# Performance work log

Measured on AMD Instinct MI355X. Metric: run time of the kernel, lower is better.

## Reference

```python
import jax, jax.numpy as jnp
import numpy as np
from jax import lax

B, T, N, F, K = 8, 16, 1024, 128, 4


def setup_inputs() -> dict:
    key = jax.random.key(0)
    k1, k2, k3, k4 = jax.random.split(key, 4)
    x = jax.random.normal(k1, (B, T, N, F), dtype=jnp.float32)
    # shift operator scaled so its spectral radius is ~1 (stable powers L^1..L^K)
    L = jax.random.normal(k2, (N, N), dtype=jnp.float32) / jnp.sqrt(jnp.float32(N))
    # xavier_uniform with relu gain: limit = gain * sqrt(6/(fan_in+fan_out))
    gain = jnp.sqrt(jnp.float32(2.0))
    lim = gain * jnp.sqrt(6.0 / (F + F))
    W = jax.random.uniform(k3, (K, F, F), dtype=jnp.float32, minval=-lim, maxval=lim)
    H = jax.random.uniform(k4, (K, F, F), dtype=jnp.float32, minval=-lim, maxval=lim)
    return {"x": x, "L": L, "W": W, "H": H}


def reference(x, L, W, H):
    """Recurrent graph-polynomial filter.

    h_t = relu( sum_{k=0}^{K-1} L^{k+1} @ (x_t @ W[k] + h_{t-1} @ H[k]) ), h_{-1}=0.
    Matches the torch loop where alpha_k starts at L and is multiplied by L each tap.
    """
    Kt = W.shape[0]
    # powers L^1 .. L^K, stacked [K, N, N]
    pows = [L]
    for _ in range(1, Kt):
        pows.append(pows[-1] @ L)
    Lp = jnp.stack(pows)

    def step(h, x_t):
        # x_t, h: [B, N, F]
        s = jnp.einsum('bnf,kfg->kbng', x_t, W) + jnp.einsum('bnf,kfg->kbng', h, H)
        z = jnp.einsum('knm,kbmg->bng', Lp, s)
        h_new = jax.nn.relu(z)
        return h_new, h_new

    xT = jnp.swapaxes(x, 0, 1)          # [T, B, N, F]
    h0 = jnp.zeros_like(x[:, 0])        # [B, N, F]
    _, outs = lax.scan(step, h0, xT)    # [T, B, N, F]
    return jnp.swapaxes(outs, 0, 1)     # [B, T, N, F]
```

## Files before the change

### kernel.cpp

```cpp
#include <hip/hip_runtime.h>
#include <stdint.h>


typedef __bf16 bf16_t;
typedef __bf16 bf16x4 __attribute__((ext_vector_type(4)));
typedef __bf16 bf16x8 __attribute__((ext_vector_type(8)));
typedef float  f32x4  __attribute__((ext_vector_type(4)));

__device__ __forceinline__ void gload_lds16(const void* g, void* l) {
    __builtin_amdgcn_global_load_lds(
        (const __attribute__((address_space(1))) void*)g,
        (__attribute__((address_space(3))) void*)l,
        16, 0, 0);
}

template<int N> __device__ __forceinline__ void wait_vmcnt() {
    if constexpr (N == 0)       asm volatile("s_waitcnt vmcnt(0)" ::: "memory");
    else if constexpr (N == 2)  asm volatile("s_waitcnt vmcnt(2)" ::: "memory");
    else if constexpr (N == 4)  asm volatile("s_waitcnt vmcnt(4)" ::: "memory");
    else if constexpr (N == 6)  asm volatile("s_waitcnt vmcnt(6)" ::: "memory");
    else if constexpr (N == 8)  asm volatile("s_waitcnt vmcnt(8)" ::: "memory");
    else                        asm volatile("s_waitcnt vmcnt(16)" ::: "memory");
}


__global__ void k_convert_x(const float* __restrict__ xin,
                            bf16_t* __restrict__ xb, int n4) {
    int i = blockIdx.x * 256 + threadIdx.x;
    int stride = gridDim.x * 256;
    for (; i < n4; i += stride) {
        float4 v = reinterpret_cast<const float4*>(xin)[i];
        bf16x4 o = { (bf16_t)v.x, (bf16_t)v.y, (bf16_t)v.z, (bf16_t)v.w };
        reinterpret_cast<bf16x4*>(xb)[i] = o;
    }
}

__global__ void k_setup_L(const float* __restrict__ L,
                          bf16_t* __restrict__ Lcat,
                          bf16_t* __restrict__ Lt) {
    int idx = blockIdx.x * 256 + threadIdx.x;
    int n = idx >> 10, m = idx & 1023;
    float v = L[idx];
    Lcat[n * 4096 + m] = (bf16_t)v;
    Lt[m * 1024 + n]   = (bf16_t)v;
}

__global__ void k_setup_WH(const float* __restrict__ W,
                           const float* __restrict__ H,
                           bf16_t* __restrict__ WHT) {
    int idx = blockIdx.x * 256 + threadIdx.x;
    int k = idx >> 14, f = (idx >> 7) & 127, g = idx & 127;
    WHT[(k * 128 + g) * 256 + f]       = (bf16_t)W[idx];
    WHT[(k * 128 + g) * 256 + 128 + f] = (bf16_t)H[idx];
}


__global__ __launch_bounds__(256)
void k_combine8(const bf16_t* __restrict__ Zp,
                bf16_t* __restrict__ h, float* __restrict__ out, int t) {
    int i = blockIdx.x * 256 + threadIdx.x;
    int n  = i >> 7;
    int c8 = (i & 127) * 8;
    size_t o = (size_t)n * 1024 + c8;
    float s[8] = {};
    #pragma unroll
    for (int z = 0; z < 8; ++z) {
        bf16x8 v = *reinterpret_cast<const bf16x8*>(Zp + (size_t)z * 1048576 + o);
        #pragma unroll
        for (int j = 0; j < 8; ++j) s[j] += (float)v[j];
    }
    bf16x8 hb;
    float4 o0, o1;
    #pragma unroll
    for (int j = 0; j < 8; ++j) {
        s[j] = fmaxf(s[j], 0.f);
        hb[j] = (bf16_t)s[j];
    }
    o0.x = s[0]; o0.y = s[1]; o0.z = s[2]; o0.w = s[3];
    o1.x = s[4]; o1.y = s[5]; o1.z = s[6]; o1.w = s[7];
    int b = c8 >> 7, g = c8 & 127;
    *reinterpret_cast<bf16x8*>(h + (size_t)b * 131072 + (size_t)n * 128 + g) = hb;
    float* op = out + (size_t)b * 2097152 + (size_t)t * 131072
                    + (size_t)n * 128 + g;
    *reinterpret_cast<float4*>(op)     = o0;
    *reinterpret_cast<float4*>(op + 4) = o1;
}

template<int BM, int BN, int GX, int GY, int GZ, int KTOT,
         int EPI, int BADDR, int ZK, int DEC, int NBUF>
__device__ __forceinline__
void gemm_body(const bf16_t* __restrict__ A, int lda,
               const bf16_t* __restrict__ BT, int ldbt,
               const bf16_t* __restrict__ B2,
               bf16_t* __restrict__ Cb, float* __restrict__ Cf,
               int ldc, int t)
{
    constexpr int BK = 64;
    constexpr int WM = BM / 2, WN = BN / 2;
    constexpr int MF = WM / 16, NF = WN / 16;
    constexpr int NT = KTOT / BK;
    constexpr int NWG = GX * GY * GZ;
    constexpr int ACH = BM * 8;
    constexpr int BCH = BN * 8;
    constexpr int LPT = (ACH + BCH) / 256;

    __shared__ __align__(16) bf16_t As[NBUF][BM * BK];
    __shared__ __align__(16) bf16_t Bs[NBUF][BN * BK];

    const int tid  = threadIdx.x;
    const int lane = tid & 63;
    const int wave = tid >> 6;
    const int wm = wave >> 1, wn = wave & 1;

    const int id  = blockIdx.x;
    const int swz = (id & 7) * (NWG / 8) + (id >> 3);
    int bx, by, bz;
    if (DEC == 0) {
        bx = swz % GX; by = (swz / GX) % GY; bz = swz / (GX * GY);
    } else {
        by = swz % GY; bz = (swz / GY) % GZ; bx = swz / (GY * GZ);
    }

    const int m0 = by * BM;
    const int c0 = bx * BN;
    const int kb_ = bz;

    const bf16_t* Ap = (EPI == 1) ? (A + kb_ * 128 * 256) : A;

    f32x4 acc[MF][NF] = {};

    auto stage = [&](int bufi, int kt) {
        const int q0 = kt * BK + (ZK > 0 ? kb_ * ZK : 0);
        #pragma unroll
        for (int i = 0; i < ACH / 256; ++i) {
            int chunk = i * 256 + tid;
            int off = chunk * 16;
            int row = off >> 7;
            int kel = ((off ^ ((row & 7) << 4)) & 127) >> 1;
            const bf16_t* src = Ap + (size_t)(m0 + row) * lda + (q0 + kel);
            gload_lds16(src, (char*)(&As[bufi][0]) + off);
        }
        #pragma unroll
        for (int i = 0; i < BCH / 256; ++i) {
            int chunk = i * 256 + tid;
            int off = chunk * 16;
            int row = off >> 7;
            int kel = ((off ^ ((row & 7) << 4)) & 127) >> 1;
            int c = c0 + row;
            const bf16_t* src;
            if (BADDR == 0) {
                src = BT + (size_t)c * ldbt + (q0 + kel);
            } else {
                int f = q0 + kel;
                if (q0 < 128) {
                    src = BT + (size_t)(c >> 10) * 2097152
                             + (size_t)t * 131072
                             + (size_t)(c & 1023) * 128 + f;
                } else {
                    src = B2 + (size_t)c * 128 + (f - 128);
                }
            }
            gload_lds16(src, (char*)(&Bs[bufi][0]) + off);
        }
    };

    auto compute = [&](int cur) {
        #pragma unroll
        for (int kk = 0; kk < 2; ++kk) {
            bf16x8 af[MF], bfr[NF];
            const int klane = (kk * 32 + (lane >> 4) * 8) * 2;
            #pragma unroll
            for (int mf = 0; mf < MF; ++mf) {
                int row = wm * WM + mf * 16 + (lane & 15);
                int bo = (row * 128 + klane) ^ ((row & 7) << 4);
                af[mf] = *reinterpret_cast<const bf16x8*>(
                             (const char*)(&As[cur][0]) + bo);
            }
            #pragma unroll
            for (int nf = 0; nf < NF; ++nf) {
                int row = wn * WN + nf * 16 + (lane & 15);
                int bo = (row * 128 + klane) ^ ((row & 7) << 4);
                bfr[nf] = *reinterpret_cast<const bf16x8*>(
                              (const char*)(&Bs[cur][0]) + bo);
            }
            #pragma unroll
            for (int mf = 0; mf < MF; ++mf)
                #pragma unroll
                for (int nf = 0; nf < NF; ++nf)
                    acc[mf][nf] = __builtin_amdgcn_mfma_f32_16x16x32_bf16(
                        af[mf], bfr[nf], acc[mf][nf], 0, 0, 0);
        }
    };

    if constexpr (NBUF == 3) {
        stage(0, 0);
        stage(1, 1);
        for (int kt = 0; kt < NT; ++kt) {
            if (kt < NT - 1) wait_vmcnt<LPT>(); else wait_vmcnt<0>();
            __builtin_amdgcn_s_barrier();
            __builtin_amdgcn_sched_barrier(0);
            if (kt + 2 < NT) stage((kt + 2) % 3, kt + 2);
            compute(kt % 3);
            __builtin_amdgcn_sched_barrier(0);
        }
    } else {
        stage(0, 0);
        stage(1, 1);
        for (int kt = 0; kt < NT; ++kt) {
            if (kt > 0 && kt + 1 < NT) {
                __builtin_amdgcn_s_barrier();
                stage((kt + 1) & 1, kt + 1);
            }
            if (kt + 1 < NT) wait_vmcnt<LPT>();
            else             wait_vmcnt<0>();
            __builtin_amdgcn_s_barrier();
            __builtin_amdgcn_sched_barrier(0);
            compute(kt & 1);
            __builtin_amdgcn_sched_barrier(0);
        }
    }

    #pragma unroll
    for (int mf = 0; mf < MF; ++mf) {
        #pragma unroll
        for (int nf = 0; nf < NF; ++nf) {
            f32x4 v = acc[mf][nf];
            int col   = c0 + wn * WN + nf * 16 + (lane & 15);
            int rbase = m0 + wm * WM + mf * 16 + ((lane >> 4) * 4);
            #pragma unroll
            for (int r = 0; r < 4; ++r) {
                int row = rbase + r;
                float val = v[r];
                if (EPI == 0) {
                    Cb[(size_t)row * ldc + col] = (bf16_t)val;
                } else if (EPI == 1) {
                    Cb[(size_t)(col >> 10) * 524288 + (size_t)row * 4096
                       + (size_t)kb_ * 1024 + (col & 1023)] = (bf16_t)val;
                } else if (EPI == 2) {
                    val = fmaxf(val, 0.f);
                    int b = col >> 7, g = col & 127;
                    Cb[(size_t)b * 131072 + (size_t)row * 128 + g] = (bf16_t)val;
                    Cf[(size_t)b * 2097152 + (size_t)t * 131072
                       + (size_t)row * 128 + g] = val;
                } else {
                    Cb[(size_t)kb_ * 1048576 + (size_t)row * 1024 + col]
                        = (bf16_t)val;
                }
            }
        }
    }
}


__global__ __launch_bounds__(256)
void k_chain(const bf16_t* __restrict__ A, const bf16_t* __restrict__ BT,
             bf16_t* __restrict__ Cb) {
    gemm_body<64, 64, 16, 16, 1, 1024, 0, 0, 0, 0, 3>(
        A, 4096, BT, 1024, nullptr, Cb, nullptr, 4096, 0);
}

__global__ __launch_bounds__(256)
void k_feat(const bf16_t* __restrict__ WHT, const bf16_t* __restrict__ xb,
            const bf16_t* __restrict__ h, bf16_t* __restrict__ Sbuf, int t) {
    gemm_body<128, 64, 128, 1, 4, 256, 1, 1, 0, 1, 3>(
        WHT, 256, xb, 0, h, Sbuf, nullptr, 0, t);
}

__global__ __launch_bounds__(256)
void k_graph(const bf16_t* __restrict__ Lcat, const bf16_t* __restrict__ Sbuf,
             bf16_t* __restrict__ Zp) {
    gemm_body<128, 128, 8, 8, 8, 512, 3, 0, 512, 0, 2>(
        Lcat, 4096, Sbuf, 4096, nullptr, Zp, nullptr, 0, 0);
}

__global__ __launch_bounds__(256)
void k_graph_ns(const bf16_t* __restrict__ Lcat, const bf16_t* __restrict__ Sbuf,
                bf16_t* __restrict__ h, float* __restrict__ out, int t) {
    gemm_body<128, 128, 8, 8, 1, 4096, 2, 0, 0, 0, 3>(
        Lcat, 4096, Sbuf, 4096, nullptr, h, out, 0, t);
}


extern "C" void kernel_launch(void* const* d_in, const int* in_sizes, int n_in,
                              void* d_out, int out_size, void* d_ws, size_t ws_size,
                              hipStream_t stream) {
    const float* x = (const float*)d_in[0];
    const float* L = (const float*)d_in[1];
    const float* W = (const float*)d_in[2];
    const float* H = (const float*)d_in[3];
    float* out = (float*)d_out;

    char* ws = (char*)d_ws;
    bf16_t* xb   = (bf16_t*)(ws);
    bf16_t* Lcat = (bf16_t*)(ws + 33554432);
    bf16_t* Lt   = (bf16_t*)(ws + 41943040);
    bf16_t* WHT  = (bf16_t*)(ws + 44040192);
    bf16_t* Sbuf = (bf16_t*)(ws + 44302336);
    bf16_t* h    = (bf16_t*)(ws + 52690944);
    bf16_t* Zp   = (bf16_t*)(ws + 54788096);
    if (ws_size < 54788096u) return;
    const bool bigws = (ws_size >= 71565312u);

    hipMemsetAsync(h, 0, 2097152, stream);
    k_convert_x<<<4096, 256, 0, stream>>>(x, xb, 16777216 / 4);
    k_setup_L <<<4096, 256, 0, stream>>>(L, Lcat, Lt);
    k_setup_WH<<<256, 256, 0, stream>>>(W, H, WHT);

    for (int p = 1; p < 4; ++p) {
        k_chain<<<256, 256, 0, stream>>>(Lcat + (p - 1) * 1024, Lt,
                                         Lcat + p * 1024);
    }

    for (int t = 0; t < 16; ++t) {
        k_feat<<<512, 256, 0, stream>>>(WHT, xb, h, Sbuf, t);
        if (bigws) {
            k_graph<<<512, 256, 0, stream>>>(Lcat, Sbuf, Zp);
            k_combine8<<<512, 256, 0, stream>>>(Zp, h, out, t);
        } else {
            k_graph_ns<<<64, 256, 0, stream>>>(Lcat, Sbuf, h, out, t);
        }
    }
}
```

Before: 503.8 us.

## Fuse split-K combine into feature GEMM and merge setup kernels

The per-step combine kernel (summing split-K partials, ReLU, writing h and output) is folded into the prologue of a new fused feature-transform kernel. That kernel builds the h tile directly in LDS and runs the W/H projection with a 3-stage async pipeline. The three setup kernels and the memset are merged into one launch. This removes 15 launches plus the global round trip of h per timestep, but the new kernel uses 256 blocks instead of 512 and recomputes the combine inside the GEMM.

```diff
diff --git a/kernel.cpp b/kernel.cpp
--- a/kernel.cpp
+++ b/kernel.cpp
@@ -17,6 +17,7 @@
 template<int N> __device__ __forceinline__ void wait_vmcnt() {
     if constexpr (N == 0)       asm volatile("s_waitcnt vmcnt(0)" ::: "memory");
     else if constexpr (N == 2)  asm volatile("s_waitcnt vmcnt(2)" ::: "memory");
+    else if constexpr (N == 3)  asm volatile("s_waitcnt vmcnt(3)" ::: "memory");
     else if constexpr (N == 4)  asm volatile("s_waitcnt vmcnt(4)" ::: "memory");
     else if constexpr (N == 6)  asm volatile("s_waitcnt vmcnt(6)" ::: "memory");
     else if constexpr (N == 8)  asm volatile("s_waitcnt vmcnt(8)" ::: "memory");
@@ -24,34 +25,30 @@
 }
 
 
-__global__ void k_convert_x(const float* __restrict__ xin,
-                            bf16_t* __restrict__ xb, int n4) {
-    int i = blockIdx.x * 256 + threadIdx.x;
-    int stride = gridDim.x * 256;
-    for (; i < n4; i += stride) {
-        float4 v = reinterpret_cast<const float4*>(xin)[i];
-        bf16x4 o = { (bf16_t)v.x, (bf16_t)v.y, (bf16_t)v.z, (bf16_t)v.w };
-        reinterpret_cast<bf16x4*>(xb)[i] = o;
-    }
-}
-
-__global__ void k_setup_L(const float* __restrict__ L,
-                          bf16_t* __restrict__ Lcat,
-                          bf16_t* __restrict__ Lt) {
-    int idx = blockIdx.x * 256 + threadIdx.x;
-    int n = idx >> 10, m = idx & 1023;
-    float v = L[idx];
-    Lcat[n * 4096 + m] = (bf16_t)v;
-    Lt[m * 1024 + n]   = (bf16_t)v;
-}
-
-__global__ void k_setup_WH(const float* __restrict__ W,
-                           const float* __restrict__ H,
-                           bf16_t* __restrict__ WHT) {
-    int idx = blockIdx.x * 256 + threadIdx.x;
-    int k = idx >> 14, f = (idx >> 7) & 127, g = idx & 127;
-    WHT[(k * 128 + g) * 256 + f]       = (bf16_t)W[idx];
-    WHT[(k * 128 + g) * 256 + 128 + f] = (bf16_t)H[idx];
+__global__ void k_setup(const float* __restrict__ x, const float* __restrict__ L,
+                        const float* __restrict__ W, const float* __restrict__ H,
+                        bf16_t* __restrict__ xb, bf16_t* __restrict__ Lcat,
+                        bf16_t* __restrict__ Lt, bf16_t* __restrict__ WHT) {
+    int bid = blockIdx.x;
+    if (bid < 4096) {
+        int idx = bid * 256 + threadIdx.x;
+        int n = idx >> 10, m = idx & 1023;
+        float v = L[idx];
+        Lcat[n * 4096 + m] = (bf16_t)v;
+        Lt[m * 1024 + n]   = (bf16_t)v;
+    } else if (bid < 4352) {
+        int idx = (bid - 4096) * 256 + threadIdx.x;
+        int k = idx >> 14, f = (idx >> 7) & 127, g = idx & 127;
+        WHT[(k * 128 + g) * 256 + f]       = (bf16_t)W[idx];
+        WHT[(k * 128 + g) * 256 + 128 + f] = (bf16_t)H[idx];
+    } else {
+        int i = (bid - 4352) * 256 + threadIdx.x;
+        for (; i < 4194304; i += 4096 * 256) {
+            float4 v = reinterpret_cast<const float4*>(x)[i];
+            bf16x4 o = { (bf16_t)v.x, (bf16_t)v.y, (bf16_t)v.z, (bf16_t)v.w };
+            reinterpret_cast<bf16x4*>(xb)[i] = o;
+        }
+    }
 }
 
 
@@ -72,10 +69,7 @@
     bf16x8 hb;
     float4 o0, o1;
     #pragma unroll
-    for (int j = 0; j < 8; ++j) {
-        s[j] = fmaxf(s[j], 0.f);
-        hb[j] = (bf16_t)s[j];
-    }
+    for (int j = 0; j < 8; ++j) { s[j] = fmaxf(s[j], 0.f); hb[j] = (bf16_t)s[j]; }
     o0.x = s[0]; o0.y = s[1]; o0.z = s[2]; o0.w = s[3];
     o1.x = s[4]; o1.y = s[5]; o1.z = s[6]; o1.w = s[7];
     int b = c8 >> 7, g = c8 & 127;
@@ -84,6 +78,163 @@
                     + (size_t)n * 128 + g;
     *reinterpret_cast<float4*>(op)     = o0;
     *reinterpret_cast<float4*>(op + 4) = o1;
+}
+
+template<bool FIRST>
+__global__ __launch_bounds__(256)
+void k_fused(const bf16_t* __restrict__ WHT, const bf16_t* __restrict__ xb,
+             const bf16_t* __restrict__ Zp, bf16_t* __restrict__ Sbuf,
+             float* __restrict__ out, int t)
+{
+    __shared__ __align__(16) bf16_t BsF[4 * 32 * 64];
+    __shared__ __align__(16) bf16_t AsF[3 * 128 * 64];
+
+    const int tid  = threadIdx.x;
+    const int lane = tid & 63;
+    const int wave = tid >> 6;
+    const int wm = wave >> 1, wn = wave & 1;
+
+    const int id = blockIdx.x;
+    const int bx = (id & 7) * 32 + (id >> 3);
+    const int c0 = bx * 32;
+    const int b  = c0 >> 10;
+    const int mb = c0 & 1023;
+
+    #pragma unroll
+    for (int ks = 0; ks < 2; ++ks) {
+        int off = tid * 16;
+        int row = off >> 7;
+        int kel = ((off ^ ((row & 7) << 4)) & 127) >> 1;
+        const bf16_t* src = xb + (size_t)b * 2097152 + (size_t)t * 131072
+                          + (size_t)(mb + row) * 128 + ks * 64 + kel;
+        gload_lds16(src, (char*)BsF + ks * 4096 + off);
+    }
+    auto stageA = [&](int bufi, int s) {
+        const int k = s >> 2, st = s & 3;
+        #pragma unroll
+        for (int i = 0; i < 4; ++i) {
+            int chunk = i * 256 + tid;
+            int off = chunk * 16;
+            int row = off >> 7;
+            int kel = ((off ^ ((row & 7) << 4)) & 127) >> 1;
+            const bf16_t* src = WHT + (size_t)(k * 128 + row) * 256
+                              + st * 64 + kel;
+            gload_lds16(src, (char*)AsF + bufi * 16384 + off);
+        }
+    };
+    stageA(0, 0);
+    stageA(1, 1);
+
+    {
+        const int r  = tid >> 3;
+        const int g0 = (tid & 7) * 16;
+        float s[16];
+        #pragma unroll
+        for (int j = 0; j < 16; ++j) s[j] = 0.f;
+        if (!FIRST) {
+            size_t o = (size_t)(mb + r) * 1024 + b * 128 + g0;
+            #pragma unroll
+            for (int z = 0; z < 8; ++z) {
+                bf16x8 v0 = *reinterpret_cast<const bf16x8*>(
+                    Zp + (size_t)z * 1048576 + o);
+                bf16x8 v1 = *reinterpret_cast<const bf16x8*>(
+                    Zp + (size_t)z * 1048576 + o + 8);
+                #pragma unroll
+                for (int j = 0; j < 8; ++j) {
+                    s[j]     += (float)v0[j];
+                    s[8 + j] += (float)v1[j];
+                }
+            }
+        }
+        bf16x8 hv[2];
+        #pragma unroll
+        for (int j = 0; j < 16; ++j) {
+            s[j] = fmaxf(s[j], 0.f);
+            hv[j >> 3][j & 7] = (bf16_t)s[j];
+        }
+        const int ks  = 2 + (g0 >> 6);
+        const int kkb = g0 & 63;
+        #pragma unroll
+        for (int j = 0; j < 2; ++j) {
+            int kk = kkb + j * 8;
+            int byte = ks * 4096 + ((r * 128 + kk * 2) ^ ((r & 7) << 4));
+            *reinterpret_cast<bf16x8*>((char*)BsF + byte) = hv[j];
+        }
+        if (!FIRST) {
+            float* op = out + (size_t)b * 2097152 + (size_t)(t - 1) * 131072
+                      + (size_t)(mb + r) * 128 + g0;
+            float4 o0, o1, o2, o3;
+            o0.x=s[0];  o0.y=s[1];  o0.z=s[2];  o0.w=s[3];
+            o1.x=s[4];  o1.y=s[5];  o1.z=s[6];  o1.w=s[7];
+            o2.x=s[8];  o2.y=s[9];  o2.z=s[10]; o2.w=s[11];
+            o3.x=s[12]; o3.y=s[13]; o3.z=s[14]; o3.w=s[15];
+            *reinterpret_cast<float4*>(op)      = o0;
+            *reinterpret_cast<float4*>(op + 4)  = o1;
+            *reinterpret_cast<float4*>(op + 8)  = o2;
+            *reinterpret_cast<float4*>(op + 12) = o3;
+        }
+    }
+    __syncthreads();
+
+    f32x4 acc[4] = {};
+    bf16x4 outv[4][4];
+    #pragma unroll
+    for (int s = 0; s < 16; ++s) {
+        if (s < 15) wait_vmcnt<4>(); else wait_vmcnt<0>();
+        __builtin_amdgcn_s_barrier();
+        __builtin_amdgcn_sched_barrier(0);
+        if (s + 2 < 16) stageA((s + 2) % 3, s + 2);
+
+        const int abase = (s % 3) * 16384;
+        const int bbase = (s & 3) * 4096;
+        #pragma unroll
+        for (int kk = 0; kk < 2; ++kk) {
+            bf16x8 af[4], bfr;
+            const int klane = (kk * 32 + (lane >> 4) * 8) * 2;
+            #pragma unroll
+            for (int mf = 0; mf < 4; ++mf) {
+                int row = wm * 64 + mf * 16 + (lane & 15);
+                int bo = (row * 128 + klane) ^ ((row & 7) << 4);
+                af[mf] = *reinterpret_cast<const bf16x8*>(
+                             (char*)AsF + abase + bo);
+            }
+            {
+                int row = wn * 16 + (lane & 15);
+                int bo = (row * 128 + klane) ^ ((row & 7) << 4);
+                bfr = *reinterpret_cast<const bf16x8*>(
+                          (char*)BsF + bbase + bo);
+            }
+            #pragma unroll
+            for (int mf = 0; mf < 4; ++mf)
+                acc[mf] = __builtin_amdgcn_mfma_f32_16x16x32_bf16(
+                    af[mf], bfr, acc[mf], 0, 0, 0);
+        }
+        __builtin_amdgcn_sched_barrier(0);
+        if ((s & 3) == 3) {
+            const int k = s >> 2;
+            #pragma unroll
+            for (int mf = 0; mf < 4; ++mf) {
+                #pragma unroll
+                for (int r2 = 0; r2 < 4; ++r2)
+                    outv[k][mf][r2] = (bf16_t)acc[mf][r2];
+                acc[mf] = (f32x4){0.f, 0.f, 0.f, 0.f};
+            }
+        }
+    }
+
+    const int col = c0 + wn * 16 + (lane & 15);
+    #pragma unroll
+    for (int k = 0; k < 4; ++k) {
+        #pragma unroll
+        for (int mf = 0; mf < 4; ++mf) {
+            int gb = wm * 64 + mf * 16 + ((lane >> 4) * 4);
+            #pragma unroll
+            for (int r2 = 0; r2 < 4; ++r2) {
+                Sbuf[(size_t)(col >> 10) * 524288 + (size_t)(gb + r2) * 4096
+                     + (size_t)k * 1024 + (col & 1023)] = outv[k][mf][r2];
+            }
+        }
+    }
 }
 
 template<int BM, int BN, int GX, int GY, int GZ, int KTOT,
@@ -301,22 +452,26 @@
     if (ws_size < 54788096u) return;
     const bool bigws = (ws_size >= 71565312u);
 
-    hipMemsetAsync(h, 0, 2097152, stream);
-    k_convert_x<<<4096, 256, 0, stream>>>(x, xb, 16777216 / 4);
-    k_setup_L <<<4096, 256, 0, stream>>>(L, Lcat, Lt);
-    k_setup_WH<<<256, 256, 0, stream>>>(W, H, WHT);
+    k_setup<<<8448, 256, 0, stream>>>(x, L, W, H, xb, Lcat, Lt, WHT);
 
     for (int p = 1; p < 4; ++p) {
         k_chain<<<256, 256, 0, stream>>>(Lcat + (p - 1) * 1024, Lt,
                                          Lcat + p * 1024);
     }
 
-    for (int t = 0; t < 16; ++t) {
-        k_feat<<<512, 256, 0, stream>>>(WHT, xb, h, Sbuf, t);
-        if (bigws) {
+    if (bigws) {
+        for (int t = 0; t < 16; ++t) {
+            if (t == 0)
+                k_fused<true><<<256, 256, 0, stream>>>(WHT, xb, Zp, Sbuf, out, t);
+            else
+                k_fused<false><<<256, 256, 0, stream>>>(WHT, xb, Zp, Sbuf, out, t);
             k_graph<<<512, 256, 0, stream>>>(Lcat, Sbuf, Zp);
-            k_combine8<<<512, 256, 0, stream>>>(Zp, h, out, t);
-        } else {
+        }
+        k_combine8<<<512, 256, 0, stream>>>(Zp, h, out, 15);
+    } else {
+        hipMemsetAsync(h, 0, 2097152, stream);
+        for (int t = 0; t < 16; ++t) {
+            k_feat<<<512, 256, 0, stream>>>(WHT, xb, h, Sbuf, t);
             k_graph_ns<<<64, 256, 0, stream>>>(Lcat, Sbuf, h, out, t);
         }
     }
```

Measured after the change: 549.6 us. 9.1% more time.

## Fuse setup kernels and compute L^3, L^4 concurrently from L^2 and its transpose

Applied to the files above, without the earlier changes.

Merges the three setup kernels (x conversion, L conversion/transpose, W/H packing) into a single launch split by block index. Replaces the three serial L-power chain GEMMs with two launches. The first computes L^2 and also writes its transpose. The second computes L^3 = L^2·L and L^4 = L^2·L^2 in parallel across a z dimension. This shortens the serial dependency chain and cuts launch count, at the cost of extra workspace and a raised threshold for the big-workspace path.

```diff
diff --git a/kernel.cpp b/kernel.cpp
--- a/kernel.cpp
+++ b/kernel.cpp
@@ -17,6 +17,7 @@
 template<int N> __device__ __forceinline__ void wait_vmcnt() {
     if constexpr (N == 0)       asm volatile("s_waitcnt vmcnt(0)" ::: "memory");
     else if constexpr (N == 2)  asm volatile("s_waitcnt vmcnt(2)" ::: "memory");
+    else if constexpr (N == 3)  asm volatile("s_waitcnt vmcnt(3)" ::: "memory");
     else if constexpr (N == 4)  asm volatile("s_waitcnt vmcnt(4)" ::: "memory");
     else if constexpr (N == 6)  asm volatile("s_waitcnt vmcnt(6)" ::: "memory");
     else if constexpr (N == 8)  asm volatile("s_waitcnt vmcnt(8)" ::: "memory");
@@ -24,34 +25,30 @@
 }
 
 
-__global__ void k_convert_x(const float* __restrict__ xin,
-                            bf16_t* __restrict__ xb, int n4) {
-    int i = blockIdx.x * 256 + threadIdx.x;
-    int stride = gridDim.x * 256;
-    for (; i < n4; i += stride) {
-        float4 v = reinterpret_cast<const float4*>(xin)[i];
-        bf16x4 o = { (bf16_t)v.x, (bf16_t)v.y, (bf16_t)v.z, (bf16_t)v.w };
-        reinterpret_cast<bf16x4*>(xb)[i] = o;
-    }
-}
-
-__global__ void k_setup_L(const float* __restrict__ L,
-                          bf16_t* __restrict__ Lcat,
-                          bf16_t* __restrict__ Lt) {
-    int idx = blockIdx.x * 256 + threadIdx.x;
-    int n = idx >> 10, m = idx & 1023;
-    float v = L[idx];
-    Lcat[n * 4096 + m] = (bf16_t)v;
-    Lt[m * 1024 + n]   = (bf16_t)v;
-}
-
-__global__ void k_setup_WH(const float* __restrict__ W,
-                           const float* __restrict__ H,
-                           bf16_t* __restrict__ WHT) {
-    int idx = blockIdx.x * 256 + threadIdx.x;
-    int k = idx >> 14, f = (idx >> 7) & 127, g = idx & 127;
-    WHT[(k * 128 + g) * 256 + f]       = (bf16_t)W[idx];
-    WHT[(k * 128 + g) * 256 + 128 + f] = (bf16_t)H[idx];
+__global__ void k_setup(const float* __restrict__ x, const float* __restrict__ L,
+                        const float* __restrict__ W, const float* __restrict__ H,
+                        bf16_t* __restrict__ xb, bf16_t* __restrict__ Lcat,
+                        bf16_t* __restrict__ Lt, bf16_t* __restrict__ WHT) {
+    int bid = blockIdx.x;
+    if (bid < 4096) {
+        int idx = bid * 256 + threadIdx.x;
+        int n = idx >> 10, m = idx & 1023;
+        float v = L[idx];
+        Lcat[n * 4096 + m] = (bf16_t)v;
+        Lt[m * 1024 + n]   = (bf16_t)v;
+    } else if (bid < 4352) {
+        int idx = (bid - 4096) * 256 + threadIdx.x;
+        int k = idx >> 14, f = (idx >> 7) & 127, g = idx & 127;
+        WHT[(k * 128 + g) * 256 + f]       = (bf16_t)W[idx];
+        WHT[(k * 128 + g) * 256 + 128 + f] = (bf16_t)H[idx];
+    } else {
+        int i = (bid - 4352) * 256 + threadIdx.x;
+        for (; i < 4194304; i += 4096 * 256) {
+            float4 v = reinterpret_cast<const float4*>(x)[i];
+            bf16x4 o = { (bf16_t)v.x, (bf16_t)v.y, (bf16_t)v.z, (bf16_t)v.w };
+            reinterpret_cast<bf16x4*>(xb)[i] = o;
+        }
+    }
 }
 
 
@@ -72,10 +69,7 @@
     bf16x8 hb;
     float4 o0, o1;
     #pragma unroll
-    for (int j = 0; j < 8; ++j) {
-        s[j] = fmaxf(s[j], 0.f);
-        hb[j] = (bf16_t)s[j];
-    }
+    for (int j = 0; j < 8; ++j) { s[j] = fmaxf(s[j], 0.f); hb[j] = (bf16_t)s[j]; }
     o0.x = s[0]; o0.y = s[1]; o0.z = s[2]; o0.w = s[3];
     o1.x = s[4]; o1.y = s[5]; o1.z = s[6]; o1.w = s[7];
     int b = c8 >> 7, g = c8 & 127;
@@ -150,6 +144,9 @@
             const bf16_t* src;
             if (BADDR == 0) {
                 src = BT + (size_t)c * ldbt + (q0 + kel);
+            } else if (BADDR == 2) {
+                const bf16_t* bt = (kb_ == 0) ? BT : B2;
+                src = bt + (size_t)c * ldbt + (q0 + kel);
             } else {
                 int f = q0 + kel;
                 if (q0 < 128) {
@@ -227,24 +224,40 @@
             f32x4 v = acc[mf][nf];
             int col   = c0 + wn * WN + nf * 16 + (lane & 15);
             int rbase = m0 + wm * WM + mf * 16 + ((lane >> 4) * 4);
-            #pragma unroll
-            for (int r = 0; r < 4; ++r) {
-                int row = rbase + r;
-                float val = v[r];
-                if (EPI == 0) {
-                    Cb[(size_t)row * ldc + col] = (bf16_t)val;
-                } else if (EPI == 1) {
-                    Cb[(size_t)(col >> 10) * 524288 + (size_t)row * 4096
-                       + (size_t)kb_ * 1024 + (col & 1023)] = (bf16_t)val;
-                } else if (EPI == 2) {
-                    val = fmaxf(val, 0.f);
-                    int b = col >> 7, g = col & 127;
-                    Cb[(size_t)b * 131072 + (size_t)row * 128 + g] = (bf16_t)val;
-                    Cf[(size_t)b * 2097152 + (size_t)t * 131072
-                       + (size_t)row * 128 + g] = val;
-                } else {
-                    Cb[(size_t)kb_ * 1048576 + (size_t)row * 1024 + col]
-                        = (bf16_t)val;
+            if constexpr (EPI == 4) {
+                bf16x4 tv;
+                #pragma unroll
+                for (int r = 0; r < 4; ++r) {
+                    float val = v[r];
+                    Cb[(size_t)(rbase + r) * 4096 + 1024 + col] = (bf16_t)val;
+                    tv[r] = (bf16_t)val;
+                }
+                *reinterpret_cast<bf16x4*>(
+                    (bf16_t*)Cf + (size_t)col * 1024 + rbase) = tv;
+            } else {
+                #pragma unroll
+                for (int r = 0; r < 4; ++r) {
+                    int row = rbase + r;
+                    float val = v[r];
+                    if (EPI == 0) {
+                        Cb[(size_t)row * ldc + col] = (bf16_t)val;
+                    } else if (EPI == 1) {
+                        Cb[(size_t)(col >> 10) * 524288 + (size_t)row * 4096
+                           + (size_t)kb_ * 1024 + (col & 1023)] = (bf16_t)val;
+                    } else if (EPI == 2) {
+                        val = fmaxf(val, 0.f);
+                        int b = col >> 7, g = col & 127;
+                        Cb[(size_t)b * 131072 + (size_t)row * 128 + g]
+                            = (bf16_t)val;
+                        Cf[(size_t)b * 2097152 + (size_t)t * 131072
+                           + (size_t)row * 128 + g] = val;
+                    } else if (EPI == 3) {
+                        Cb[(size_t)kb_ * 1048576 + (size_t)row * 1024 + col]
+                            = (bf16_t)val;
+                    } else {
+                        Cb[(size_t)row * 4096 + 2048 + kb_ * 1024 + col]
+                            = (bf16_t)val;
+                    }
                 }
             }
         }
@@ -257,6 +270,20 @@
              bf16_t* __restrict__ Cb) {
     gemm_body<64, 64, 16, 16, 1, 1024, 0, 0, 0, 0, 3>(
         A, 4096, BT, 1024, nullptr, Cb, nullptr, 4096, 0);
+}
+
+__global__ __launch_bounds__(256)
+void k_chain1(const bf16_t* __restrict__ Lcat, const bf16_t* __restrict__ Lt,
+              bf16_t* __restrict__ Cb, bf16_t* __restrict__ Lt2) {
+    gemm_body<64, 64, 16, 16, 1, 1024, 4, 0, 0, 0, 3>(
+        Lcat, 4096, Lt, 1024, nullptr, Cb, (float*)Lt2, 0, 0);
+}
+
+__global__ __launch_bounds__(256)
+void k_chain2(const bf16_t* __restrict__ A, const bf16_t* __restrict__ Lt,
+              const bf16_t* __restrict__ Lt2, bf16_t* __restrict__ Cb) {
+    gemm_body<64, 64, 16, 16, 2, 1024, 6, 2, 0, 0, 3>(
+        A, 4096, Lt, 1024, Lt2, Cb, nullptr, 0, 0);
 }
 
 __global__ __launch_bounds__(256)
@@ -298,25 +325,28 @@
     bf16_t* Sbuf = (bf16_t*)(ws + 44302336);
     bf16_t* h    = (bf16_t*)(ws + 52690944);
     bf16_t* Zp   = (bf16_t*)(ws + 54788096);
+    bf16_t* Lt2  = (bf16_t*)(ws + 71565312);
     if (ws_size < 54788096u) return;
-    const bool bigws = (ws_size >= 71565312u);
+    const bool bigws = (ws_size >= 73662464u);
 
     hipMemsetAsync(h, 0, 2097152, stream);
-    k_convert_x<<<4096, 256, 0, stream>>>(x, xb, 16777216 / 4);
-    k_setup_L <<<4096, 256, 0, stream>>>(L, Lcat, Lt);
-    k_setup_WH<<<256, 256, 0, stream>>>(W, H, WHT);
-
-    for (int p = 1; p < 4; ++p) {
-        k_chain<<<256, 256, 0, stream>>>(Lcat + (p - 1) * 1024, Lt,
-                                         Lcat + p * 1024);
-    }
-
-    for (int t = 0; t < 16; ++t) {
-        k_feat<<<512, 256, 0, stream>>>(WHT, xb, h, Sbuf, t);
-        if (bigws) {
+    k_setup<<<8448, 256, 0, stream>>>(x, L, W, H, xb, Lcat, Lt, WHT);
+
+    if (bigws) {
+        k_chain1<<<256, 256, 0, stream>>>(Lcat, Lt, Lcat, Lt2);
+        k_chain2<<<512, 256, 0, stream>>>(Lcat + 1024, Lt, Lt2, Lcat);
+        for (int t = 0; t < 16; ++t) {
+            k_feat<<<512, 256, 0, stream>>>(WHT, xb, h, Sbuf, t);
             k_graph<<<512, 256, 0, stream>>>(Lcat, Sbuf, Zp);
             k_combine8<<<512, 256, 0, stream>>>(Zp, h, out, t);
-        } else {
+        }
+    } else {
+        for (int p = 1; p < 4; ++p) {
+            k_chain<<<256, 256, 0, stream>>>(Lcat + (p - 1) * 1024, Lt,
+                                             Lcat + p * 1024);
+        }
+        for (int t = 0; t < 16; ++t) {
+            k_feat<<<512, 256, 0, stream>>>(WHT, xb, h, Sbuf, t);
             k_graph_ns<<<64, 256, 0, stream>>>(Lcat, Sbuf, h, out, t);
         }
     }
```

Measured after the change: 493.9 us (median of 2 runs). -2.0%, faster.
